# Performance work log

Hardware: AMD Instinct MI355X
Metric: run time of the kernel (lower is better)

## Reference

```python
import jax, jax.numpy as jnp
import numpy as np

GROUP = 128

def dequantize_groupwise(vals, scales, group_size=GROUP):
    # vals: [rows, cols] int, scales: [rows, cols//group_size]
    rows, cols = vals.shape
    groups = cols // group_size
    v = vals.astype(jnp.float32).reshape(rows, groups, group_size)
    return (v * scales[:, :, None]).reshape(rows, cols)

def setup_inputs() -> dict:
    key = jax.random.key(0)
    ks = jax.random.split(key, 8)
    B, S, D_IN, D_OUT, R = 4, 2048, 4096, 4096, 256
    return {
        "x": jax.random.normal(ks[0], (B, S, D_IN), dtype=jnp.float32),
        "q_values": jax.random.randint(ks[1], (D_OUT, D_IN), 0, 16, dtype=jnp.int32),
        "q_scales": jax.random.uniform(ks[2], (D_OUT, D_IN // GROUP), dtype=jnp.float32),
        "l_values": jax.random.randint(ks[3], (D_OUT, R), 0, 16, dtype=jnp.int32),
        "l_scales": jax.random.uniform(ks[4], (D_OUT, R // GROUP), dtype=jnp.float32),
        "r_values": jax.random.randint(ks[5], (R, D_IN), 0, 16, dtype=jnp.int32),
        "r_scales": jax.random.uniform(ks[6], (R, D_IN // GROUP), dtype=jnp.float32),
        "bias": jax.random.normal(ks[7], (D_OUT,), dtype=jnp.float32),
    }

def reference(x, q_values, q_scales, l_values, l_scales, r_values, r_scales, bias):
    # Dequantize (groupwise scale along last dim); unpack is identity (packed_bits=None)
    q = dequantize_groupwise(q_values, q_scales)   # [out, in]
    l = dequantize_groupwise(l_values, l_scales)   # [out, rank]
    r = dequantize_groupwise(r_values, r_scales)   # [rank, in]
    orig_shape = x.shape
    xf = x.reshape(-1, orig_shape[-1])             # [N, in]
    xr = xf @ r.T                                  # [N, rank]
    out = xf @ q.T + xr @ l.T + bias               # [N, out]
    return out.reshape(*orig_shape[:-1], q.shape[0])
```

## Files before the change

kernel.cpp:

```cpp
#include <hip/hip_runtime.h>

#define D_IN  4096
#define D_OUT 4096
#define RANK  256
#define KCAT  (D_IN + RANK)

typedef _Float16 h4 __attribute__((ext_vector_type(4)));
typedef _Float16 h8 __attribute__((ext_vector_type(8)));
typedef float    f4 __attribute__((ext_vector_type(4)));

__device__ __forceinline__ void gload16(const void* g, void* l) {
  __builtin_amdgcn_global_load_lds(
      (const __attribute__((address_space(1))) void*)g,
      (__attribute__((address_space(3))) void*)l, 16, 0, 0);
}


__global__ __launch_bounds__(256) void k_dequant_w(
    const int* __restrict__ qv, const float* __restrict__ qs,
    const int* __restrict__ lv, const float* __restrict__ ls,
    _Float16* __restrict__ W) {
  int row = blockIdx.y;
  int c4 = blockIdx.x * 256 + threadIdx.x;
  if (c4 >= KCAT / 4) return;
  int col = c4 * 4;
  int4 v; float s;
  if (col < D_IN) {
    v = *(const int4*)(qv + (size_t)row * D_IN + col);
    s = qs[row * (D_IN / 128) + (col >> 7)];
  } else {
    int lc = col - D_IN;
    v = *(const int4*)(lv + (size_t)row * RANK + lc);
    s = ls[row * (RANK / 128) + (lc >> 7)];
  }
  h4 h;
  h[0] = (_Float16)((float)v.x * s);
  h[1] = (_Float16)((float)v.y * s);
  h[2] = (_Float16)((float)v.z * s);
  h[3] = (_Float16)((float)v.w * s);
  *(h4*)(W + (size_t)row * KCAT + col) = h;
}

__global__ __launch_bounds__(256) void k_dequant_r(
    const int* __restrict__ rv, const float* __restrict__ rs,
    _Float16* __restrict__ R) {
  int row = blockIdx.y;
  int c4 = blockIdx.x * 256 + threadIdx.x;
  int col = c4 * 4;
  int4 v = *(const int4*)(rv + (size_t)row * D_IN + col);
  float s = rs[row * (D_IN / 128) + (col >> 7)];
  h4 h;
  h[0] = (_Float16)((float)v.x * s);
  h[1] = (_Float16)((float)v.y * s);
  h[2] = (_Float16)((float)v.z * s);
  h[3] = (_Float16)((float)v.w * s);
  *(h4*)(R + (size_t)row * D_IN + col) = h;
}

__global__ __launch_bounds__(256) void k_convert_x(
    const float* __restrict__ x, _Float16* __restrict__ X, int total4) {
  int i = blockIdx.x * 256 + threadIdx.x;
  if (i >= total4) return;
  f4 v = *(const f4*)(x + (size_t)i * 4);
  int row = i >> 10;
  int c4  = i & 1023;
  h4 h;
  h[0] = (_Float16)v[0]; h[1] = (_Float16)v[1];
  h[2] = (_Float16)v[2]; h[3] = (_Float16)v[3];
  *(h4*)(X + (size_t)row * KCAT + c4 * 4) = h;
}

template<int BM, int BN, int MF, int NF, bool OUT_F16, bool ADD_BIAS>
__global__ __launch_bounds__(256) void k_gemm_bt(
    const _Float16* __restrict__ A, int lda,
    const _Float16* __restrict__ B, int ldb,
    void* __restrict__ Cv, int ldc,
    const float* __restrict__ bias,
    int K, int grid_n) {
  constexpr int WM = MF * 16, WN = NF * 16;
  __shared__ _Float16 As[BM][32];
  __shared__ _Float16 Bs[BN][32];

  int bid = blockIdx.x;
  { int q = gridDim.x >> 3; bid = (bid & 7) * q + (bid >> 3); }
  int bm = bid / grid_n, bn = bid % grid_n;

  int tid  = threadIdx.x;
  int lane = tid & 63, wave = tid >> 6;
  int wr = wave >> 1, wc = wave & 1;

  int trow = tid >> 2;
  int tcol = (tid & 3) * 8;
  const _Float16* ga = A + (size_t)(bm * BM + trow) * lda + tcol;
  const _Float16* gb = B + (size_t)(bn * BN + trow) * ldb + tcol;

  f4 acc[MF][NF] = {};

  int fr = lane & 15;
  int fk = (lane >> 4) * 8;

  for (int k0 = 0; k0 < K; k0 += 32) {
#pragma unroll
    for (int p = 0; p < BM / 64; ++p)
      gload16(ga + (size_t)p * 64 * lda + k0, &As[p * 64 + trow][tcol]);
#pragma unroll
    for (int p = 0; p < BN / 64; ++p)
      gload16(gb + (size_t)p * 64 * ldb + k0, &Bs[p * 64 + trow][tcol]);
    __syncthreads();

    h8 a[MF], b[NF];
#pragma unroll
    for (int m = 0; m < MF; ++m)
      a[m] = *(const h8*)&As[wr * WM + m * 16 + fr][fk];
#pragma unroll
    for (int n = 0; n < NF; ++n)
      b[n] = *(const h8*)&Bs[wc * WN + n * 16 + fr][fk];
#pragma unroll
    for (int m = 0; m < MF; ++m)
#pragma unroll
      for (int n = 0; n < NF; ++n)
        acc[m][n] = __builtin_amdgcn_mfma_f32_16x16x32_f16(a[m], b[n], acc[m][n], 0, 0, 0);
    __syncthreads();
  }

  int cr = (lane >> 4) * 4;
  int cc = lane & 15;
#pragma unroll
  for (int m = 0; m < MF; ++m) {
#pragma unroll
    for (int n = 0; n < NF; ++n) {
      int col = bn * BN + wc * WN + n * 16 + cc;
      float bv = ADD_BIAS ? bias[col] : 0.f;
#pragma unroll
      for (int r = 0; r < 4; ++r) {
        int row = bm * BM + wr * WM + m * 16 + cr + r;
        float val = acc[m][n][r] + bv;
        if (OUT_F16) ((_Float16*)Cv)[(size_t)row * ldc + col] = (_Float16)val;
        else         ((float*)Cv)[(size_t)row * ldc + col]    = val;
      }
    }
  }
}

__global__ __launch_bounds__(512, 2) void k_gemm256(
    const _Float16* __restrict__ A,
    const _Float16* __restrict__ B,
    float* __restrict__ C,
    const float* __restrict__ bias) {
  constexpr int LDA = KCAT, LDB = KCAT, LDC = D_OUT;
  constexpr int NT = KCAT / 64;
  constexpr int GRID_N = D_OUT / 256;
  __shared__ _Float16 smem[2 * 4 * 8192];

  int bid = blockIdx.x;
  { int q = gridDim.x >> 3; bid = (bid & 7) * q + (bid >> 3); }
  const int bm = bid / GRID_N, bn = bid % GRID_N;

  const int tid  = threadIdx.x;
  const int lane = tid & 63, wave = tid >> 6;
  const int wr = wave >> 2;
  const int wc = wave & 3;

  const int fr   = lane & 15;
  const int kgrp = lane >> 4;
  const int xorv = fr & 7;
  const int seg0 = ((0 | kgrp) ^ xorv) * 8;
  const int seg1 = ((4 | kgrp) ^ xorv) * 8;

  const int srow = tid >> 3;
  const int scol = ((tid & 7) ^ (srow & 7)) * 8;
  const _Float16* gA = A + (size_t)(bm * 256 + srow) * LDA + scol;
  const _Float16* gB = B + (size_t)(bn * 256 + srow) * LDB + scol;

  f4 acc[8][4] = {};
  h8 a_lo[4][2], a_hi[4][2], b01[2][2], b23[2][2];

  auto stA = [&](int buf, int h, int t) {
    const _Float16* g = gA + (size_t)h * 128 * LDA + t * 64;
    _Float16* l = smem + (buf * 4 + h) * 8192 + tid * 8;
    gload16(g, l);
    gload16(g + (size_t)64 * LDA, l + 4096);
  };
  auto stB = [&](int buf, int h, int t) {
    const _Float16* g = gB + (size_t)h * 128 * LDB + t * 64;
    _Float16* l = smem + (buf * 4 + 2 + h) * 8192 + tid * 8;
    gload16(g, l);
    gload16(g + (size_t)64 * LDB, l + 4096);
  };
  auto rdA = [&](h8 (&dst)[4][2], int buf, int mbase) {
    const _Float16* p = smem + (buf * 4 + wr) * 8192 + fr * 64;
#pragma unroll
    for (int mm = 0; mm < 4; ++mm) {
      dst[mm][0] = *(const h8*)(p + (mbase + mm) * 1024 + seg0);
      dst[mm][1] = *(const h8*)(p + (mbase + mm) * 1024 + seg1);
    }
  };
  auto rdB = [&](h8 (&dst)[2][2], int buf, int nbase) {
    const _Float16* p = smem + (buf * 4 + 2 + (wc >> 1)) * 8192
                      + ((wc & 1) * 64 + fr) * 64;
#pragma unroll
    for (int nn = 0; nn < 2; ++nn) {
      dst[nn][0] = *(const h8*)(p + (nbase + nn) * 1024 + seg0);
      dst[nn][1] = *(const h8*)(p + (nbase + nn) * 1024 + seg1);
    }
  };

#define QUAD(AF, BF, MO, NO)                                                   \
  __builtin_amdgcn_s_setprio(1);                                               \
  _Pragma("unroll")                                                            \
  for (int mm = 0; mm < 4; ++mm)                                               \
    _Pragma("unroll")                                                          \
    for (int nn = 0; nn < 2; ++nn) {                                           \
      acc[MO + mm][NO + nn] = __builtin_amdgcn_mfma_f32_16x16x32_f16(          \
          AF[mm][0], BF[nn][0], acc[MO + mm][NO + nn], 0, 0, 0);               \
      acc[MO + mm][NO + nn] = __builtin_amdgcn_mfma_f32_16x16x32_f16(          \
          AF[mm][1], BF[nn][1], acc[MO + mm][NO + nn], 0, 0, 0);               \
    }                                                                          \
  __builtin_amdgcn_s_setprio(0);

#define BAR() __builtin_amdgcn_s_barrier()
#define LGKM(N) asm volatile("s_waitcnt lgkmcnt(" #N ")" ::: "memory")
#define VMC(N)  asm volatile("s_waitcnt vmcnt(" #N ")" ::: "memory")

  stA(0, 0, 0); stA(0, 1, 0); stB(0, 0, 0); stB(0, 1, 0);
  stB(1, 0, 1); stB(1, 1, 1);
  VMC(4);
  BAR();
  rdA(a_lo, 0, 0); rdB(b01, 0, 0);

  auto tile = [&](int t, int buf) {
    const int nbuf = buf ^ 1;
    rdB(b23, buf, 2);
    if (t + 1 < NT) stA(nbuf, 0, t + 1);
    BAR();
    LGKM(4);
    QUAD(a_lo, b01, 0, 0);
    BAR();
    rdA(a_hi, buf, 4);
    if (t + 1 < NT) stA(nbuf, 1, t + 1);
    BAR();
    LGKM(8);
    QUAD(a_lo, b23, 0, 2);
    BAR();
    if (t + 2 < NT) stB(buf, 0, t + 2);
    BAR();
    LGKM(0);
    QUAD(a_hi, b01, 4, 0);
    BAR();
    if (t + 2 < NT) {
      stB(buf, 1, t + 2);
      VMC(4);
    } else {
      VMC(0);
    }
    BAR();
    if (t + 1 < NT) { rdA(a_lo, nbuf, 0); rdB(b01, nbuf, 0); }
    QUAD(a_hi, b23, 4, 2);
    BAR();
  };

  for (int tt = 0; tt < NT; tt += 2) {
    tile(tt, 0);
    tile(tt + 1, 1);
  }

  const int crow = bm * 256 + wr * 128 + kgrp * 4;
  const int ccol = bn * 256 + wc * 64 + fr;
#pragma unroll
  for (int n = 0; n < 4; ++n) {
    const int col = ccol + n * 16;
    const float bv = bias[col];
#pragma unroll
    for (int m = 0; m < 8; ++m) {
      const int row0 = crow + m * 16;
#pragma unroll
      for (int r = 0; r < 4; ++r)
        C[(size_t)(row0 + r) * LDC + col] = acc[m][n][r] + bv;
    }
  }
#undef QUAD
#undef BAR
#undef LGKM
#undef VMC
}

extern "C" void kernel_launch(void* const* d_in, const int* in_sizes, int n_in,
                              void* d_out, int out_size, void* d_ws, size_t ws_size,
                              hipStream_t stream) {
  const float* x    = (const float*)d_in[0];
  const int*   qv   = (const int*)d_in[1];
  const float* qs   = (const float*)d_in[2];
  const int*   lv   = (const int*)d_in[3];
  const float* ls   = (const float*)d_in[4];
  const int*   rv   = (const int*)d_in[5];
  const float* rs   = (const float*)d_in[6];
  const float* bias = (const float*)d_in[7];

  int M = in_sizes[0] / D_IN;

  char* ws = (char*)d_ws;
  _Float16* Xcat = (_Float16*)ws;
  _Float16* Wcat = (_Float16*)(ws + (size_t)M * KCAT * 2);
  _Float16* Rh   = (_Float16*)(ws + (size_t)(M + D_OUT) * KCAT * 2);

  k_dequant_w<<<dim3((KCAT / 4 + 255) / 256, D_OUT), 256, 0, stream>>>(qv, qs, lv, ls, Wcat);
  k_dequant_r<<<dim3(D_IN / 4 / 256, RANK), 256, 0, stream>>>(rv, rs, Rh);
  int total4 = M * (D_IN / 4);
  k_convert_x<<<(total4 + 255) / 256, 256, 0, stream>>>(x, Xcat, total4);

  k_gemm_bt<64, 64, 2, 2, true, false><<<(M / 64) * (RANK / 64), 256, 0, stream>>>(
      Xcat, KCAT, Rh, D_IN, (void*)(Xcat + D_IN), KCAT, nullptr, D_IN, RANK / 64);

  k_gemm256<<<(M / 256) * (D_OUT / 256), 512, 0, stream>>>(
      Xcat, Wcat, (float*)d_out, bias);
}
```

Baseline: 569.4 us.

## Switch main GEMM to 32x32x16 MFMA and widen preprocessing kernels to 8 elements

The main 256x256 GEMM moves from 16x16x32 MFMA tiles to 32x32x16 MFMA tiles, with new LDS fragment read patterns, 16-wide accumulators and a matching epilogue row mapping. The larger MFMA tile means fewer instructions and less LDS fragment traffic per FLOP. The dequant and convert kernels now handle 8 elements per thread with 16-byte stores, and the combined W dequant is split into separate q and l kernels. The new swizzled fragment reads and the epilogue mapping must match the 32x32 MFMA layout exactly, and the 16-wide accumulators raise register pressure.

```diff
diff --git a/kernel.cpp b/kernel.cpp
--- a/kernel.cpp
+++ b/kernel.cpp
@@ -5,9 +5,9 @@
 #define RANK  256
 #define KCAT  (D_IN + RANK)
 
-typedef _Float16 h4 __attribute__((ext_vector_type(4)));
 typedef _Float16 h8 __attribute__((ext_vector_type(8)));
 typedef float    f4 __attribute__((ext_vector_type(4)));
+typedef float    f16v __attribute__((ext_vector_type(16)));
 
 __device__ __forceinline__ void gload16(const void* g, void* l) {
   __builtin_amdgcn_global_load_lds(
@@ -15,59 +15,65 @@
       (__attribute__((address_space(3))) void*)l, 16, 0, 0);
 }
 
-
-__global__ __launch_bounds__(256) void k_dequant_w(
+__device__ __forceinline__ h8 dq8(int4 v0, int4 v1, float s) {
+  h8 h;
+  h[0] = (_Float16)((float)v0.x * s);
+  h[1] = (_Float16)((float)v0.y * s);
+  h[2] = (_Float16)((float)v0.z * s);
+  h[3] = (_Float16)((float)v0.w * s);
+  h[4] = (_Float16)((float)v1.x * s);
+  h[5] = (_Float16)((float)v1.y * s);
+  h[6] = (_Float16)((float)v1.z * s);
+  h[7] = (_Float16)((float)v1.w * s);
+  return h;
+}
+
+
+__global__ __launch_bounds__(256) void k_dequant_q(
     const int* __restrict__ qv, const float* __restrict__ qs,
+    _Float16* __restrict__ W) {
+  int i = blockIdx.x * 256 + threadIdx.x;
+  int row = i >> 9, c8 = (i & 511) << 3;
+  const int* p = qv + (size_t)row * D_IN + c8;
+  int4 v0 = *(const int4*)p, v1 = *(const int4*)(p + 4);
+  float s = qs[row * (D_IN / 128) + (c8 >> 7)];
+  *(h8*)(W + (size_t)row * KCAT + c8) = dq8(v0, v1, s);
+}
+
+__global__ __launch_bounds__(256) void k_dequant_l(
     const int* __restrict__ lv, const float* __restrict__ ls,
     _Float16* __restrict__ W) {
-  int row = blockIdx.y;
-  int c4 = blockIdx.x * 256 + threadIdx.x;
-  if (c4 >= KCAT / 4) return;
-  int col = c4 * 4;
-  int4 v; float s;
-  if (col < D_IN) {
-    v = *(const int4*)(qv + (size_t)row * D_IN + col);
-    s = qs[row * (D_IN / 128) + (col >> 7)];
-  } else {
-    int lc = col - D_IN;
-    v = *(const int4*)(lv + (size_t)row * RANK + lc);
-    s = ls[row * (RANK / 128) + (lc >> 7)];
-  }
-  h4 h;
-  h[0] = (_Float16)((float)v.x * s);
-  h[1] = (_Float16)((float)v.y * s);
-  h[2] = (_Float16)((float)v.z * s);
-  h[3] = (_Float16)((float)v.w * s);
-  *(h4*)(W + (size_t)row * KCAT + col) = h;
+  int i = blockIdx.x * 256 + threadIdx.x;
+  int row = i >> 5, c8 = (i & 31) << 3;
+  const int* p = lv + (size_t)row * RANK + c8;
+  int4 v0 = *(const int4*)p, v1 = *(const int4*)(p + 4);
+  float s = ls[row * (RANK / 128) + (c8 >> 7)];
+  *(h8*)(W + (size_t)row * KCAT + D_IN + c8) = dq8(v0, v1, s);
 }
 
 __global__ __launch_bounds__(256) void k_dequant_r(
     const int* __restrict__ rv, const float* __restrict__ rs,
     _Float16* __restrict__ R) {
-  int row = blockIdx.y;
-  int c4 = blockIdx.x * 256 + threadIdx.x;
-  int col = c4 * 4;
-  int4 v = *(const int4*)(rv + (size_t)row * D_IN + col);
-  float s = rs[row * (D_IN / 128) + (col >> 7)];
-  h4 h;
-  h[0] = (_Float16)((float)v.x * s);
-  h[1] = (_Float16)((float)v.y * s);
-  h[2] = (_Float16)((float)v.z * s);
-  h[3] = (_Float16)((float)v.w * s);
-  *(h4*)(R + (size_t)row * D_IN + col) = h;
+  int i = blockIdx.x * 256 + threadIdx.x;
+  int row = i >> 9, c8 = (i & 511) << 3;
+  const int* p = rv + (size_t)row * D_IN + c8;
+  int4 v0 = *(const int4*)p, v1 = *(const int4*)(p + 4);
+  float s = rs[row * (D_IN / 128) + (c8 >> 7)];
+  *(h8*)(R + (size_t)row * D_IN + c8) = dq8(v0, v1, s);
 }
 
 __global__ __launch_bounds__(256) void k_convert_x(
-    const float* __restrict__ x, _Float16* __restrict__ X, int total4) {
+    const float* __restrict__ x, _Float16* __restrict__ X) {
   int i = blockIdx.x * 256 + threadIdx.x;
-  if (i >= total4) return;
-  f4 v = *(const f4*)(x + (size_t)i * 4);
-  int row = i >> 10;
-  int c4  = i & 1023;
-  h4 h;
-  h[0] = (_Float16)v[0]; h[1] = (_Float16)v[1];
-  h[2] = (_Float16)v[2]; h[3] = (_Float16)v[3];
-  *(h4*)(X + (size_t)row * KCAT + c4 * 4) = h;
+  int row = i >> 9, c8 = (i & 511) << 3;
+  const float* p = x + (size_t)row * D_IN + c8;
+  f4 v0 = *(const f4*)p, v1 = *(const f4*)(p + 4);
+  h8 h;
+  h[0] = (_Float16)v0[0]; h[1] = (_Float16)v0[1];
+  h[2] = (_Float16)v0[2]; h[3] = (_Float16)v0[3];
+  h[4] = (_Float16)v1[0]; h[5] = (_Float16)v1[1];
+  h[6] = (_Float16)v1[2]; h[7] = (_Float16)v1[3];
+  *(h8*)(X + (size_t)row * KCAT + c8) = h;
 }
 
 template<int BM, int BN, int MF, int NF, bool OUT_F16, bool ADD_BIAS>
@@ -161,19 +167,18 @@
   const int wr = wave >> 2;
   const int wc = wave & 3;
 
-  const int fr   = lane & 15;
-  const int kgrp = lane >> 4;
-  const int xorv = fr & 7;
-  const int seg0 = ((0 | kgrp) ^ xorv) * 8;
-  const int seg1 = ((4 | kgrp) ^ xorv) * 8;
+  const int fr32  = lane & 31;
+  const int khalf = lane >> 5;
+  const int xorv  = fr32 & 7;
 
   const int srow = tid >> 3;
   const int scol = ((tid & 7) ^ (srow & 7)) * 8;
   const _Float16* gA = A + (size_t)(bm * 256 + srow) * LDA + scol;
   const _Float16* gB = B + (size_t)(bn * 256 + srow) * LDB + scol;
 
-  f4 acc[8][4] = {};
-  h8 a_lo[4][2], a_hi[4][2], b01[2][2], b23[2][2];
+  f16v acc[4][2] = {};
+  h8 a_lo[2][4], a_hi[2][4];
+  h8 b0[4], b1[4];
 
   auto stA = [&](int buf, int h, int t) {
     const _Float16* g = gA + (size_t)h * 128 * LDA + t * 64;
@@ -187,35 +192,32 @@
     gload16(g, l);
     gload16(g + (size_t)64 * LDB, l + 4096);
   };
-  auto rdA = [&](h8 (&dst)[4][2], int buf, int mbase) {
-    const _Float16* p = smem + (buf * 4 + wr) * 8192 + fr * 64;
-#pragma unroll
-    for (int mm = 0; mm < 4; ++mm) {
-      dst[mm][0] = *(const h8*)(p + (mbase + mm) * 1024 + seg0);
-      dst[mm][1] = *(const h8*)(p + (mbase + mm) * 1024 + seg1);
+  auto rdA = [&](h8 (&dst)[2][4], int buf, int mbase) {
+    const _Float16* p = smem + (buf * 4 + wr) * 8192;
+#pragma unroll
+    for (int mm = 0; mm < 2; ++mm) {
+      const _Float16* rp = p + ((mbase + mm) * 32 + fr32) * 64;
+#pragma unroll
+      for (int ks = 0; ks < 4; ++ks)
+        dst[mm][ks] = *(const h8*)(rp + (((ks * 2 + khalf) ^ xorv) << 3));
     }
   };
-  auto rdB = [&](h8 (&dst)[2][2], int buf, int nbase) {
-    const _Float16* p = smem + (buf * 4 + 2 + (wc >> 1)) * 8192
-                      + ((wc & 1) * 64 + fr) * 64;
-#pragma unroll
-    for (int nn = 0; nn < 2; ++nn) {
-      dst[nn][0] = *(const h8*)(p + (nbase + nn) * 1024 + seg0);
-      dst[nn][1] = *(const h8*)(p + (nbase + nn) * 1024 + seg1);
-    }
+  auto rdB = [&](h8 (&dst)[4], int buf, int nt) {
+    const _Float16* rp = smem + (buf * 4 + 2 + (wc >> 1)) * 8192
+                       + ((wc & 1) * 64 + nt * 32 + fr32) * 64;
+#pragma unroll
+    for (int ks = 0; ks < 4; ++ks)
+      dst[ks] = *(const h8*)(rp + (((ks * 2 + khalf) ^ xorv) << 3));
   };
 
 #define QUAD(AF, BF, MO, NO)                                                   \
   __builtin_amdgcn_s_setprio(1);                                               \
   _Pragma("unroll")                                                            \
-  for (int mm = 0; mm < 4; ++mm)                                               \
+  for (int ks = 0; ks < 4; ++ks)                                               \
     _Pragma("unroll")                                                          \
-    for (int nn = 0; nn < 2; ++nn) {                                           \
-      acc[MO + mm][NO + nn] = __builtin_amdgcn_mfma_f32_16x16x32_f16(          \
-          AF[mm][0], BF[nn][0], acc[MO + mm][NO + nn], 0, 0, 0);               \
-      acc[MO + mm][NO + nn] = __builtin_amdgcn_mfma_f32_16x16x32_f16(          \
-          AF[mm][1], BF[nn][1], acc[MO + mm][NO + nn], 0, 0, 0);               \
-    }                                                                          \
+    for (int mm = 0; mm < 2; ++mm)                                             \
+      acc[MO + mm][NO] = __builtin_amdgcn_mfma_f32_32x32x16_f16(               \
+          AF[mm][ks], BF[ks], acc[MO + mm][NO], 0, 0, 0);                      \
   __builtin_amdgcn_s_setprio(0);
 
 #define BAR() __builtin_amdgcn_s_barrier()
@@ -226,26 +228,26 @@
   stB(1, 0, 1); stB(1, 1, 1);
   VMC(4);
   BAR();
-  rdA(a_lo, 0, 0); rdB(b01, 0, 0);
+  rdA(a_lo, 0, 0); rdB(b0, 0, 0);
 
   auto tile = [&](int t, int buf) {
     const int nbuf = buf ^ 1;
-    rdB(b23, buf, 2);
+    rdB(b1, buf, 1);
     if (t + 1 < NT) stA(nbuf, 0, t + 1);
     BAR();
     LGKM(4);
-    QUAD(a_lo, b01, 0, 0);
-    BAR();
-    rdA(a_hi, buf, 4);
+    QUAD(a_lo, b0, 0, 0);
+    BAR();
+    rdA(a_hi, buf, 2);
     if (t + 1 < NT) stA(nbuf, 1, t + 1);
     BAR();
     LGKM(8);
-    QUAD(a_lo, b23, 0, 2);
+    QUAD(a_lo, b1, 0, 1);
     BAR();
     if (t + 2 < NT) stB(buf, 0, t + 2);
     BAR();
     LGKM(0);
-    QUAD(a_hi, b01, 4, 0);
+    QUAD(a_hi, b0, 2, 0);
     BAR();
     if (t + 2 < NT) {
       stB(buf, 1, t + 2);
@@ -254,8 +256,8 @@
       VMC(0);
     }
     BAR();
-    if (t + 1 < NT) { rdA(a_lo, nbuf, 0); rdB(b01, nbuf, 0); }
-    QUAD(a_hi, b23, 4, 2);
+    if (t + 1 < NT) { rdA(a_lo, nbuf, 0); rdB(b0, nbuf, 0); }
+    QUAD(a_hi, b1, 2, 1);
     BAR();
   };
 
@@ -264,18 +266,20 @@
     tile(tt + 1, 1);
   }
 
-  const int crow = bm * 256 + wr * 128 + kgrp * 4;
-  const int ccol = bn * 256 + wc * 64 + fr;
-#pragma unroll
-  for (int n = 0; n < 4; ++n) {
-    const int col = ccol + n * 16;
+  const int crow = bm * 256 + wr * 128 + (khalf << 2);
+  const int ccol = bn * 256 + wc * 64 + fr32;
+#pragma unroll
+  for (int n = 0; n < 2; ++n) {
+    const int col = ccol + n * 32;
     const float bv = bias[col];
 #pragma unroll
-    for (int m = 0; m < 8; ++m) {
-      const int row0 = crow + m * 16;
-#pragma unroll
-      for (int r = 0; r < 4; ++r)
-        C[(size_t)(row0 + r) * LDC + col] = acc[m][n][r] + bv;
+    for (int m = 0; m < 4; ++m) {
+      const int row0 = crow + m * 32;
+#pragma unroll
+      for (int r = 0; r < 16; ++r) {
+        const int row = row0 + (r & 3) + ((r >> 2) << 3);
+        C[(size_t)row * LDC + col] = acc[m][n][r] + bv;
+      }
     }
   }
 #undef QUAD
@@ -303,10 +307,10 @@
   _Float16* Wcat = (_Float16*)(ws + (size_t)M * KCAT * 2);
   _Float16* Rh   = (_Float16*)(ws + (size_t)(M + D_OUT) * KCAT * 2);
 
-  k_dequant_w<<<dim3((KCAT / 4 + 255) / 256, D_OUT), 256, 0, stream>>>(qv, qs, lv, ls, Wcat);
-  k_dequant_r<<<dim3(D_IN / 4 / 256, RANK), 256, 0, stream>>>(rv, rs, Rh);
-  int total4 = M * (D_IN / 4);
-  k_convert_x<<<(total4 + 255) / 256, 256, 0, stream>>>(x, Xcat, total4);
+  k_dequant_q<<<D_OUT * (D_IN / 8) / 256, 256, 0, stream>>>(qv, qs, Wcat);
+  k_dequant_l<<<D_OUT * (RANK / 8) / 256, 256, 0, stream>>>(lv, ls, Wcat);
+  k_dequant_r<<<RANK * (D_IN / 8) / 256, 256, 0, stream>>>(rv, rs, Rh);
+  k_convert_x<<<M * (D_IN / 8) / 256, 256, 0, stream>>>(x, Xcat);
 
   k_gemm_bt<64, 64, 2, 2, true, false><<<(M / 64) * (RANK / 64), 256, 0, stream>>>(
       Xcat, KCAT, Rh, D_IN, (void*)(Xcat + D_IN), KCAT, nullptr, D_IN, RANK / 64);
```

Result: slower. 617.9 us (+8.5%).

## Fold low-rank product into dequantized weight before main GEMM

Applied to the files above, without the earlier changes.

Instead of computing x@R^T per token and concatenating it along K, the code precomputes W = Q + L@R as a single fp16 weight matrix via a small GEMM fused with Q dequantization. The main GEMM then runs over K=D_IN instead of D_IN+RANK and the per-batch rank projection GEMM disappears. The trade is an extra 4096x4096x256 weight-side GEMM, an uncoalesced transpose of R, and rounding of L@R into fp16 together with Q, which changes numerics slightly.

```diff
diff --git a/kernel.cpp b/kernel.cpp
--- a/kernel.cpp
+++ b/kernel.cpp
@@ -3,9 +3,7 @@
 #define D_IN  4096
 #define D_OUT 4096
 #define RANK  256
-#define KCAT  (D_IN + RANK)
-
-typedef _Float16 h4 __attribute__((ext_vector_type(4)));
+
 typedef _Float16 h8 __attribute__((ext_vector_type(8)));
 typedef float    f4 __attribute__((ext_vector_type(4)));
 
@@ -15,75 +13,71 @@
       (__attribute__((address_space(3))) void*)l, 16, 0, 0);
 }
 
-
-__global__ __launch_bounds__(256) void k_dequant_w(
+__device__ __forceinline__ h8 dq8(int4 v0, int4 v1, float s) {
+  h8 h;
+  h[0] = (_Float16)((float)v0.x * s);
+  h[1] = (_Float16)((float)v0.y * s);
+  h[2] = (_Float16)((float)v0.z * s);
+  h[3] = (_Float16)((float)v0.w * s);
+  h[4] = (_Float16)((float)v1.x * s);
+  h[5] = (_Float16)((float)v1.y * s);
+  h[6] = (_Float16)((float)v1.z * s);
+  h[7] = (_Float16)((float)v1.w * s);
+  return h;
+}
+
+
+__global__ __launch_bounds__(256) void k_dequant_l2(
+    const int* __restrict__ lv, const float* __restrict__ ls,
+    _Float16* __restrict__ L) {
+  int i = blockIdx.x * 256 + threadIdx.x;
+  int row = i >> 5, c8 = (i & 31) << 3;
+  const int* p = lv + (size_t)row * RANK + c8;
+  int4 v0 = *(const int4*)p, v1 = *(const int4*)(p + 4);
+  float s = ls[row * (RANK / 128) + (c8 >> 7)];
+  *(h8*)(L + (size_t)row * RANK + c8) = dq8(v0, v1, s);
+}
+
+__global__ __launch_bounds__(256) void k_transpose_r(
+    const int* __restrict__ rv, const float* __restrict__ rs,
+    _Float16* __restrict__ RT) {
+  int i = blockIdx.x * 256 + threadIdx.x;
+  int c8 = (i >> 12) << 3;
+  int irow = i & 4095;
+  h8 h;
+#pragma unroll
+  for (int j = 0; j < 8; ++j) {
+    int k = c8 + j;
+    float s = rs[k * (D_IN / 128) + (irow >> 7)];
+    h[j] = (_Float16)((float)rv[(size_t)k * D_IN + irow] * s);
+  }
+  *(h8*)(RT + (size_t)irow * RANK + c8) = h;
+}
+
+__global__ __launch_bounds__(256) void k_convert_x(
+    const float* __restrict__ x, _Float16* __restrict__ X) {
+  int i = blockIdx.x * 256 + threadIdx.x;
+  const float* p = x + (size_t)i * 8;
+  f4 v0 = *(const f4*)p, v1 = *(const f4*)(p + 4);
+  h8 h;
+  h[0] = (_Float16)v0[0]; h[1] = (_Float16)v0[1];
+  h[2] = (_Float16)v0[2]; h[3] = (_Float16)v0[3];
+  h[4] = (_Float16)v1[0]; h[5] = (_Float16)v1[1];
+  h[6] = (_Float16)v1[2]; h[7] = (_Float16)v1[3];
+  *(h8*)(X + (size_t)i * 8) = h;
+}
+
+__global__ __launch_bounds__(256) void k_wfull(
+    const _Float16* __restrict__ A,
+    const _Float16* __restrict__ B,
     const int* __restrict__ qv, const float* __restrict__ qs,
-    const int* __restrict__ lv, const float* __restrict__ ls,
     _Float16* __restrict__ W) {
-  int row = blockIdx.y;
-  int c4 = blockIdx.x * 256 + threadIdx.x;
-  if (c4 >= KCAT / 4) return;
-  int col = c4 * 4;
-  int4 v; float s;
-  if (col < D_IN) {
-    v = *(const int4*)(qv + (size_t)row * D_IN + col);
-    s = qs[row * (D_IN / 128) + (col >> 7)];
-  } else {
-    int lc = col - D_IN;
-    v = *(const int4*)(lv + (size_t)row * RANK + lc);
-    s = ls[row * (RANK / 128) + (lc >> 7)];
-  }
-  h4 h;
-  h[0] = (_Float16)((float)v.x * s);
-  h[1] = (_Float16)((float)v.y * s);
-  h[2] = (_Float16)((float)v.z * s);
-  h[3] = (_Float16)((float)v.w * s);
-  *(h4*)(W + (size_t)row * KCAT + col) = h;
-}
-
-__global__ __launch_bounds__(256) void k_dequant_r(
-    const int* __restrict__ rv, const float* __restrict__ rs,
-    _Float16* __restrict__ R) {
-  int row = blockIdx.y;
-  int c4 = blockIdx.x * 256 + threadIdx.x;
-  int col = c4 * 4;
-  int4 v = *(const int4*)(rv + (size_t)row * D_IN + col);
-  float s = rs[row * (D_IN / 128) + (col >> 7)];
-  h4 h;
-  h[0] = (_Float16)((float)v.x * s);
-  h[1] = (_Float16)((float)v.y * s);
-  h[2] = (_Float16)((float)v.z * s);
-  h[3] = (_Float16)((float)v.w * s);
-  *(h4*)(R + (size_t)row * D_IN + col) = h;
-}
-
-__global__ __launch_bounds__(256) void k_convert_x(
-    const float* __restrict__ x, _Float16* __restrict__ X, int total4) {
-  int i = blockIdx.x * 256 + threadIdx.x;
-  if (i >= total4) return;
-  f4 v = *(const f4*)(x + (size_t)i * 4);
-  int row = i >> 10;
-  int c4  = i & 1023;
-  h4 h;
-  h[0] = (_Float16)v[0]; h[1] = (_Float16)v[1];
-  h[2] = (_Float16)v[2]; h[3] = (_Float16)v[3];
-  *(h4*)(X + (size_t)row * KCAT + c4 * 4) = h;
-}
-
-template<int BM, int BN, int MF, int NF, bool OUT_F16, bool ADD_BIAS>
-__global__ __launch_bounds__(256) void k_gemm_bt(
-    const _Float16* __restrict__ A, int lda,
-    const _Float16* __restrict__ B, int ldb,
-    void* __restrict__ Cv, int ldc,
-    const float* __restrict__ bias,
-    int K, int grid_n) {
-  constexpr int WM = MF * 16, WN = NF * 16;
-  __shared__ _Float16 As[BM][32];
-  __shared__ _Float16 Bs[BN][32];
+  __shared__ _Float16 As[64][32];
+  __shared__ _Float16 Bs[64][32];
 
   int bid = blockIdx.x;
   { int q = gridDim.x >> 3; bid = (bid & 7) * q + (bid >> 3); }
-  int bm = bid / grid_n, bn = bid % grid_n;
+  int bm = bid >> 6, bn = bid & 63;
 
   int tid  = threadIdx.x;
   int lane = tid & 63, wave = tid >> 6;
@@ -91,34 +85,28 @@
 
   int trow = tid >> 2;
   int tcol = (tid & 3) * 8;
-  const _Float16* ga = A + (size_t)(bm * BM + trow) * lda + tcol;
-  const _Float16* gb = B + (size_t)(bn * BN + trow) * ldb + tcol;
-
-  f4 acc[MF][NF] = {};
-
+  const _Float16* ga = A + (size_t)(bm * 64 + trow) * RANK + tcol;
+  const _Float16* gb = B + (size_t)(bn * 64 + trow) * RANK + tcol;
+
+  f4 acc[2][2] = {};
   int fr = lane & 15;
   int fk = (lane >> 4) * 8;
 
-  for (int k0 = 0; k0 < K; k0 += 32) {
-#pragma unroll
-    for (int p = 0; p < BM / 64; ++p)
-      gload16(ga + (size_t)p * 64 * lda + k0, &As[p * 64 + trow][tcol]);
-#pragma unroll
-    for (int p = 0; p < BN / 64; ++p)
-      gload16(gb + (size_t)p * 64 * ldb + k0, &Bs[p * 64 + trow][tcol]);
+  for (int k0 = 0; k0 < RANK; k0 += 32) {
+    gload16(ga + k0, &As[trow][tcol]);
+    gload16(gb + k0, &Bs[trow][tcol]);
     __syncthreads();
-
-    h8 a[MF], b[NF];
-#pragma unroll
-    for (int m = 0; m < MF; ++m)
-      a[m] = *(const h8*)&As[wr * WM + m * 16 + fr][fk];
-#pragma unroll
-    for (int n = 0; n < NF; ++n)
-      b[n] = *(const h8*)&Bs[wc * WN + n * 16 + fr][fk];
-#pragma unroll
-    for (int m = 0; m < MF; ++m)
-#pragma unroll
-      for (int n = 0; n < NF; ++n)
+    h8 a[2], b[2];
+#pragma unroll
+    for (int m = 0; m < 2; ++m)
+      a[m] = *(const h8*)&As[wr * 32 + m * 16 + fr][fk];
+#pragma unroll
+    for (int n = 0; n < 2; ++n)
+      b[n] = *(const h8*)&Bs[wc * 32 + n * 16 + fr][fk];
+#pragma unroll
+    for (int m = 0; m < 2; ++m)
+#pragma unroll
+      for (int n = 0; n < 2; ++n)
         acc[m][n] = __builtin_amdgcn_mfma_f32_16x16x32_f16(a[m], b[n], acc[m][n], 0, 0, 0);
     __syncthreads();
   }
@@ -126,20 +114,18 @@
   int cr = (lane >> 4) * 4;
   int cc = lane & 15;
 #pragma unroll
-  for (int m = 0; m < MF; ++m) {
-#pragma unroll
-    for (int n = 0; n < NF; ++n) {
-      int col = bn * BN + wc * WN + n * 16 + cc;
-      float bv = ADD_BIAS ? bias[col] : 0.f;
+  for (int m = 0; m < 2; ++m)
+#pragma unroll
+    for (int n = 0; n < 2; ++n) {
+      int col = bn * 64 + wc * 32 + n * 16 + cc;
 #pragma unroll
       for (int r = 0; r < 4; ++r) {
-        int row = bm * BM + wr * WM + m * 16 + cr + r;
-        float val = acc[m][n][r] + bv;
-        if (OUT_F16) ((_Float16*)Cv)[(size_t)row * ldc + col] = (_Float16)val;
-        else         ((float*)Cv)[(size_t)row * ldc + col]    = val;
+        int row = bm * 64 + wr * 32 + m * 16 + cr + r;
+        float qd = (float)qv[(size_t)row * D_IN + col]
+                 * qs[row * (D_IN / 128) + (col >> 7)];
+        W[(size_t)row * D_IN + col] = (_Float16)(acc[m][n][r] + qd);
       }
     }
-  }
 }
 
 __global__ __launch_bounds__(512, 2) void k_gemm256(
@@ -147,8 +133,8 @@
     const _Float16* __restrict__ B,
     float* __restrict__ C,
     const float* __restrict__ bias) {
-  constexpr int LDA = KCAT, LDB = KCAT, LDC = D_OUT;
-  constexpr int NT = KCAT / 64;
+  constexpr int LDA = D_IN, LDB = D_IN, LDC = D_OUT;
+  constexpr int NT = D_IN / 64;
   constexpr int GRID_N = D_OUT / 256;
   __shared__ _Float16 smem[2 * 4 * 8192];
 
@@ -299,18 +285,17 @@
   int M = in_sizes[0] / D_IN;
 
   char* ws = (char*)d_ws;
-  _Float16* Xcat = (_Float16*)ws;
-  _Float16* Wcat = (_Float16*)(ws + (size_t)M * KCAT * 2);
-  _Float16* Rh   = (_Float16*)(ws + (size_t)(M + D_OUT) * KCAT * 2);
-
-  k_dequant_w<<<dim3((KCAT / 4 + 255) / 256, D_OUT), 256, 0, stream>>>(qv, qs, lv, ls, Wcat);
-  k_dequant_r<<<dim3(D_IN / 4 / 256, RANK), 256, 0, stream>>>(rv, rs, Rh);
-  int total4 = M * (D_IN / 4);
-  k_convert_x<<<(total4 + 255) / 256, 256, 0, stream>>>(x, Xcat, total4);
-
-  k_gemm_bt<64, 64, 2, 2, true, false><<<(M / 64) * (RANK / 64), 256, 0, stream>>>(
-      Xcat, KCAT, Rh, D_IN, (void*)(Xcat + D_IN), KCAT, nullptr, D_IN, RANK / 64);
+  _Float16* Xh = (_Float16*)ws;
+  _Float16* Wf = (_Float16*)(ws + (size_t)M * D_IN * 2);
+  _Float16* Lh = Wf + (size_t)D_OUT * D_IN;
+  _Float16* RT = Lh + (size_t)D_OUT * RANK;
+
+  k_dequant_l2<<<D_OUT * (RANK / 8) / 256, 256, 0, stream>>>(lv, ls, Lh);
+  k_transpose_r<<<D_IN * (RANK / 8) / 256, 256, 0, stream>>>(rv, rs, RT);
+  k_convert_x<<<M * (D_IN / 8) / 256, 256, 0, stream>>>(x, Xh);
+
+  k_wfull<<<(D_OUT / 64) * (D_IN / 64), 256, 0, stream>>>(Lh, RT, qv, qs, Wf);
 
   k_gemm256<<<(M / 256) * (D_OUT / 256), 512, 0, stream>>>(
-      Xcat, Wcat, (float*)d_out, bias);
-}
+      Xh, Wf, (float*)d_out, bias);
+}
```

Result: faster. 554.2 us (-2.7%).
